# Performance work log

Hardware: AMD Instinct MI355X
Metric: run time of the kernel (lower is better)

## Reference

```python
import jax, jax.numpy as jnp
import numpy as np

N_NODES = 40000
N_EDGES = 640000
D_FEAT = 128


def setup_inputs() -> dict:
    key = jax.random.key(0)
    k1, k2, k3, k4 = jax.random.split(key, 4)
    rows = jax.random.randint(k1, (N_EDGES,), 0, N_NODES, dtype=jnp.int32)
    cols = jax.random.randint(k2, (N_EDGES,), 0, N_NODES, dtype=jnp.int32)
    vals = jax.random.uniform(k3, (N_EDGES,), dtype=jnp.float32)
    annotations = jax.random.normal(k4, (N_NODES, D_FEAT), dtype=jnp.float32)
    return {"rows": rows, "cols": cols, "vals": vals, "annotations": annotations}


def reference(rows, cols, vals, annotations):
    # out = adjacent @ annotations, with adjacent given in COO form:
    # adjacent[rows[e], cols[e]] = vals[e].
    # SpMM as gather -> scale -> segment_sum over destination rows.
    gathered = annotations[cols] * vals[:, None]          # [E, d]
    out = jax.ops.segment_sum(gathered, rows, num_segments=N_NODES)  # [N, d]
    return out
```

## Files before the change

kernel.cpp:

```cpp
#include <hip/hip_runtime.h>


constexpr int N_NODES = 40000;
constexpr int N_EDGES = 640000;
constexpr int D_FEAT  = 128;
constexpr int CAP     = 32;
constexpr int OVF_CAP = 16384;

constexpr size_t WS_CURSOR = 0;
constexpr size_t WS_OVFCNT = 160000;
constexpr size_t WS_OVF    = 160256;
constexpr size_t WS_ANNB   = 422400;
constexpr size_t WS_PAIRS  = 10662400;
constexpr size_t WS_NEEDED = 20902400;

__device__ __forceinline__ unsigned f2b_rne(float f) {
    unsigned b = __float_as_uint(f);
    return (b + 0x7fffu + ((b >> 16) & 1u)) >> 16;
}

__global__ __launch_bounds__(256) void convert_kernel(
    const float* __restrict__ ann, uint2* __restrict__ annb)
{
    int t = blockIdx.x * blockDim.x + threadIdx.x;
    if (t < N_NODES * D_FEAT / 4) {
        float4 f = reinterpret_cast<const float4*>(ann)[t];
        uint2 o;
        o.x = f2b_rne(f.x) | (f2b_rne(f.y) << 16);
        o.y = f2b_rne(f.z) | (f2b_rne(f.w) << 16);
        annb[t] = o;
    }
}

__device__ __forceinline__ void scatter_one(
    int r, int c, float v, int* cursor, int2* pairs,
    int* ovfcnt, int4* ovf)
{
    int slot = atomicAdd(&cursor[r], 1);
    if (slot < CAP) {
        pairs[r * CAP + slot] = make_int2(c, __float_as_int(v));
    } else {
        int o = atomicAdd(ovfcnt, 1);
        if (o < OVF_CAP) ovf[o] = make_int4(r, c, __float_as_int(v), 0);
    }
}

__global__ __launch_bounds__(256) void scatter_kernel(
    const int*   __restrict__ rows,
    const int*   __restrict__ cols,
    const float* __restrict__ vals,
    int* __restrict__ cursor, int2* __restrict__ pairs,
    int* __restrict__ ovfcnt, int4* __restrict__ ovf)
{
    int t = blockIdx.x * blockDim.x + threadIdx.x;
    if (t < N_EDGES / 4) {
        int4   r4 = reinterpret_cast<const int4*>(rows)[t];
        int4   c4 = reinterpret_cast<const int4*>(cols)[t];
        float4 v4 = reinterpret_cast<const float4*>(vals)[t];
        scatter_one(r4.x, c4.x, v4.x, cursor, pairs, ovfcnt, ovf);
        scatter_one(r4.y, c4.y, v4.y, cursor, pairs, ovfcnt, ovf);
        scatter_one(r4.z, c4.z, v4.z, cursor, pairs, ovfcnt, ovf);
        scatter_one(r4.w, c4.w, v4.w, cursor, pairs, ovfcnt, ovf);
    }
}

__global__ __launch_bounds__(256) void pull_kernel(
    const unsigned* __restrict__ annb,
    const int*      __restrict__ cursor,
    const int2*     __restrict__ pairs,
    float*          __restrict__ out)
{
    int r    = (blockIdx.x * blockDim.x + threadIdx.x) >> 6;
    int lane = threadIdx.x & 63;
    if (r >= N_NODES) return;

    int cnt = cursor[r];
    cnt = cnt > CAP ? CAP : cnt;

    int2 pr = make_int2(0, 0);
    if (lane < cnt) pr = pairs[r * CAP + lane];

    float2 acc = make_float2(0.f, 0.f);
    int nb = (cnt + 7) & ~7;
    for (int j = 0; j < nb; j += 8) {
        #pragma unroll
        for (int k = 0; k < 8; k++) {
            int      c = __shfl(pr.x, j + k, 64);
            float    v = __int_as_float(__shfl(pr.y, j + k, 64));
            unsigned p = annb[c * (D_FEAT / 2) + lane];
            float a0 = __uint_as_float(p << 16);
            float a1 = __uint_as_float(p & 0xffff0000u);
            acc.x += v * a0;
            acc.y += v * a1;
        }
    }
    ((float2*)out)[(size_t)r * (D_FEAT / 2) + lane] = acc;
}

__global__ __launch_bounds__(256) void post_kernel(
    const float* __restrict__ ann,
    const int*   __restrict__ ovfcnt,
    const int4*  __restrict__ ovf,
    float*       __restrict__ out)
{
    int gid  = blockIdx.x * blockDim.x + threadIdx.x;
    int h    = gid >> 5;
    int lane = gid & 31;
    int n = *ovfcnt;
    n = n > OVF_CAP ? OVF_CAP : n;
    const int n_halves = (gridDim.x * blockDim.x) >> 5;
    for (int i = h; i < n; i += n_halves) {
        int4  e = ovf[i];
        float v = __int_as_float(e.z);
        float4 a = reinterpret_cast<const float4*>(ann)[(size_t)e.y * (D_FEAT / 4) + lane];
        float* o = out + (size_t)e.x * D_FEAT + lane * 4;
        unsafeAtomicAdd(o + 0, v * a.x);
        unsafeAtomicAdd(o + 1, v * a.y);
        unsafeAtomicAdd(o + 2, v * a.z);
        unsafeAtomicAdd(o + 3, v * a.w);
    }
}

__global__ __launch_bounds__(256) void spmm_scatter_kernel(
    const int*   __restrict__ rows,
    const int*   __restrict__ cols,
    const float* __restrict__ vals,
    const float* __restrict__ ann,
    float*       __restrict__ out)
{
    int t = blockIdx.x * blockDim.x + threadIdx.x;
    int e = t >> 5;
    if (e >= N_EDGES) return;
    int lane = t & 31;
    int   r = rows[e];
    int   c = cols[e];
    float v = vals[e];
    float4 a = reinterpret_cast<const float4*>(ann)[(size_t)c * (D_FEAT / 4) + lane];
    float* o = out + (size_t)r * D_FEAT + lane * 4;
    unsafeAtomicAdd(o + 0, v * a.x);
    unsafeAtomicAdd(o + 1, v * a.y);
    unsafeAtomicAdd(o + 2, v * a.z);
    unsafeAtomicAdd(o + 3, v * a.w);
}

extern "C" void kernel_launch(void* const* d_in, const int* in_sizes, int n_in,
                              void* d_out, int out_size, void* d_ws, size_t ws_size,
                              hipStream_t stream) {
    const int*   rows = (const int*)  d_in[0];
    const int*   cols = (const int*)  d_in[1];
    const float* vals = (const float*)d_in[2];
    const float* ann  = (const float*)d_in[3];
    float*       out  = (float*)      d_out;

    if (ws_size < WS_NEEDED) {
        hipMemsetAsync(out, 0, (size_t)out_size * sizeof(float), stream);
        const long long total_threads = (long long)N_EDGES * 32;
        spmm_scatter_kernel<<<dim3((unsigned)((total_threads + 255) / 256)),
                              dim3(256), 0, stream>>>(rows, cols, vals, ann, out);
        return;
    }

    char*     ws     = (char*)d_ws;
    int*      cursor = (int*)     (ws + WS_CURSOR);
    int*      ovfcnt = (int*)     (ws + WS_OVFCNT);
    int4*     ovf    = (int4*)    (ws + WS_OVF);
    unsigned* annb   = (unsigned*)(ws + WS_ANNB);
    int2*     pairs  = (int2*)    (ws + WS_PAIRS);

    hipMemsetAsync(cursor, 0, WS_OVF, stream);

    convert_kernel<<<dim3((N_NODES * D_FEAT / 4 + 255) / 256), dim3(256), 0, stream>>>(
        ann, (uint2*)annb);
    scatter_kernel<<<dim3((N_EDGES / 4 + 255) / 256), dim3(256), 0, stream>>>(
        rows, cols, vals, cursor, pairs, ovfcnt, ovf);

    const long long pull_threads = (long long)N_NODES * 64;
    pull_kernel<<<dim3((unsigned)((pull_threads + 255) / 256)), dim3(256), 0, stream>>>(
        annb, cursor, pairs, out);

    post_kernel<<<dim3(32), dim3(256), 0, stream>>>(ann, ovfcnt, ovf, out);
}
```

Measured before the change: 142.7 us.

## Fuse scatter and bf16 convert into one launch, add nontemporal loads/stores

Merges the edge-scatter and the fp32-to-bf16 feature conversion into a single build kernel, with block ranges split between the two roles so they run concurrently and one launch is saved. The scatter now handles one edge per thread instead of four. Edge loads, pair stores and the final output stores use nontemporal hints so streaming data stays out of cache and leaves room for the gathered features. Risks: the finer-grained scatter raises thread count, and nontemporal pair stores could hurt the pull kernel if those pairs would otherwise have stayed in cache.

Result: no change. 143.1 us (+0.3%).

```diff
diff --git a/kernel.cpp b/kernel.cpp
--- a/kernel.cpp
+++ b/kernel.cpp
@@ -6,6 +6,11 @@
 constexpr int D_FEAT  = 128;
 constexpr int CAP     = 32;
 constexpr int OVF_CAP = 16384;
+
+constexpr int SCAT_BLKS   = N_EDGES / 256;
+constexpr int CONV_BLKS   = 1250;
+constexpr int CONV_STRIDE = CONV_BLKS * 256;
+constexpr int CONV_TOTAL  = N_NODES * D_FEAT / 4;
 
 constexpr size_t WS_CURSOR = 0;
 constexpr size_t WS_OVFCNT = 160000;
@@ -19,48 +24,40 @@
     return (b + 0x7fffu + ((b >> 16) & 1u)) >> 16;
 }
 
-__global__ __launch_bounds__(256) void convert_kernel(
-    const float* __restrict__ ann, uint2* __restrict__ annb)
-{
-    int t = blockIdx.x * blockDim.x + threadIdx.x;
-    if (t < N_NODES * D_FEAT / 4) {
-        float4 f = reinterpret_cast<const float4*>(ann)[t];
-        uint2 o;
-        o.x = f2b_rne(f.x) | (f2b_rne(f.y) << 16);
-        o.y = f2b_rne(f.z) | (f2b_rne(f.w) << 16);
-        annb[t] = o;
-    }
-}
-
-__device__ __forceinline__ void scatter_one(
-    int r, int c, float v, int* cursor, int2* pairs,
-    int* ovfcnt, int4* ovf)
-{
-    int slot = atomicAdd(&cursor[r], 1);
-    if (slot < CAP) {
-        pairs[r * CAP + slot] = make_int2(c, __float_as_int(v));
-    } else {
-        int o = atomicAdd(ovfcnt, 1);
-        if (o < OVF_CAP) ovf[o] = make_int4(r, c, __float_as_int(v), 0);
-    }
-}
-
-__global__ __launch_bounds__(256) void scatter_kernel(
+__global__ __launch_bounds__(256) void build_kernel(
     const int*   __restrict__ rows,
     const int*   __restrict__ cols,
     const float* __restrict__ vals,
+    const float* __restrict__ ann,
     int* __restrict__ cursor, int2* __restrict__ pairs,
-    int* __restrict__ ovfcnt, int4* __restrict__ ovf)
+    int* __restrict__ ovfcnt, int4* __restrict__ ovf,
+    uint2* __restrict__ annb)
 {
-    int t = blockIdx.x * blockDim.x + threadIdx.x;
-    if (t < N_EDGES / 4) {
-        int4   r4 = reinterpret_cast<const int4*>(rows)[t];
-        int4   c4 = reinterpret_cast<const int4*>(cols)[t];
-        float4 v4 = reinterpret_cast<const float4*>(vals)[t];
-        scatter_one(r4.x, c4.x, v4.x, cursor, pairs, ovfcnt, ovf);
-        scatter_one(r4.y, c4.y, v4.y, cursor, pairs, ovfcnt, ovf);
-        scatter_one(r4.z, c4.z, v4.z, cursor, pairs, ovfcnt, ovf);
-        scatter_one(r4.w, c4.w, v4.w, cursor, pairs, ovfcnt, ovf);
+    if (blockIdx.x < (unsigned)SCAT_BLKS) {
+        int e = blockIdx.x * 256 + threadIdx.x;
+        int   r = __builtin_nontemporal_load(&rows[e]);
+        int   c = __builtin_nontemporal_load(&cols[e]);
+        float v = __builtin_nontemporal_load(&vals[e]);
+        int slot = atomicAdd(&cursor[r], 1);
+        if (slot < CAP) {
+            int2 pr = make_int2(c, __float_as_int(v));
+            long long pbits;
+            __builtin_memcpy(&pbits, &pr, 8);
+            __builtin_nontemporal_store(
+                pbits, reinterpret_cast<long long*>(&pairs[r * CAP + slot]));
+        } else {
+            int o = atomicAdd(ovfcnt, 1);
+            if (o < OVF_CAP) ovf[o] = make_int4(r, c, __float_as_int(v), 0);
+        }
+    } else {
+        int t = (blockIdx.x - SCAT_BLKS) * 256 + threadIdx.x;
+        for (; t < CONV_TOTAL; t += CONV_STRIDE) {
+            float4 f = reinterpret_cast<const float4*>(ann)[t];
+            uint2 o;
+            o.x = f2b_rne(f.x) | (f2b_rne(f.y) << 16);
+            o.y = f2b_rne(f.z) | (f2b_rne(f.w) << 16);
+            annb[t] = o;
+        }
     }
 }
 
@@ -94,7 +91,11 @@
             acc.y += v * a1;
         }
     }
-    ((float2*)out)[(size_t)r * (D_FEAT / 2) + lane] = acc;
+    long long obits;
+    __builtin_memcpy(&obits, &acc, 8);
+    __builtin_nontemporal_store(
+        obits, reinterpret_cast<long long*>(
+                   &((float2*)out)[(size_t)r * (D_FEAT / 2) + lane]));
 }
 
 __global__ __launch_bounds__(256) void post_kernel(
@@ -169,10 +170,8 @@
 
     hipMemsetAsync(cursor, 0, WS_OVF, stream);
 
-    convert_kernel<<<dim3((N_NODES * D_FEAT / 4 + 255) / 256), dim3(256), 0, stream>>>(
-        ann, (uint2*)annb);
-    scatter_kernel<<<dim3((N_EDGES / 4 + 255) / 256), dim3(256), 0, stream>>>(
-        rows, cols, vals, cursor, pairs, ovfcnt, ovf);
+    build_kernel<<<dim3(SCAT_BLKS + CONV_BLKS), dim3(256), 0, stream>>>(
+        rows, cols, vals, ann, cursor, pairs, ovfcnt, ovf, (uint2*)annb);
 
     const long long pull_threads = (long long)N_NODES * 64;
     pull_kernel<<<dim3((unsigned)((pull_threads + 255) / 256)), dim3(256), 0, stream>>>(
```
